# Kernel tuning notes

Hardware: AMD Instinct MI355X
Metric: run time of the kernel (lower is better)

## Reference

```python
import jax, jax.numpy as jnp
import numpy as np

SIM_THRESHOLD = 0.5   # similarity_threshold
LAMBDA = 0.1          # lambda_weight default


def setup_inputs() -> dict:
    key = jax.random.key(0)
    ks = jax.random.split(key, 8)
    B, T, C, P = 8, 1024, 1024, 100
    return {
        "attention_scores": jax.random.normal(ks[0], (B, T, T), jnp.float32),
        "context": jax.random.normal(ks[1], (B, C), jnp.float32),
        "triggers": jax.random.normal(ks[2], (P, C), jnp.float32),
        "biases": jax.random.uniform(ks[3], (P, T, T), jnp.float32),
        "confidences": jnp.ones((P,), jnp.float32),
        "W1": jax.random.normal(ks[4], (2 * C, C), jnp.float32) * (1.0 / np.sqrt(2 * C)),
        "b1": jnp.zeros((C,), jnp.float32),
        "W2": jax.random.normal(ks[5], (C,), jnp.float32) * (1.0 / np.sqrt(C)),
        "b2": jnp.zeros((1,), jnp.float32),
    }


def reference(attention_scores, context, triggers, biases, confidences, W1, b1, W2, b2):
    C = context.shape[-1]
    # combined = cat([context, trigger]) @ W1 == context @ W1[:C] + trigger @ W1[C:]
    ctx_h = context @ W1[:C]              # (B, C)
    trg_h = triggers @ W1[C:]             # (P, C)
    h = jax.nn.relu(ctx_h[:, None, :] + trg_h[None, :, :] + b1)   # (B, P, C)
    logits = h @ W2 + b2[0]               # (B, P)
    scores = jax.nn.sigmoid(logits).mean(axis=0)                  # (P,) mean over batch
    # match: only patterns with score > threshold contribute, weighted by score*confidence
    weights = jnp.where(scores > SIM_THRESHOLD, scores * confidences, 0.0)  # (P,)
    reasoning_bias = jnp.einsum("p,pij->ij", weights, biases)     # (T, T)
    return attention_scores + LAMBDA * reasoning_bias[None, :, :]
```

## Files before the change

kernel.cpp:

```cpp
#include <hip/hip_runtime.h>
#include <hip/hip_bf16.h>
#include <math.h>

#define BD 8
#define TD 1024
#define CD 1024
#define PD 100
#define KS 16
#define KW (CD / KS)
#define LAMBDA 0.1f
#define SIM_THR 0.5f

typedef float f2 __attribute__((ext_vector_type(2)));
typedef float f4 __attribute__((ext_vector_type(4)));

__device__ float    g_pctx[KS][BD][CD];
__device__ float    g_ptrg[KS][PD][CD];
__device__ float    g_wd[PD];
__device__ float    g_wc[PD];
__device__ unsigned g_poff[PD];
__device__ int      g_nnz;

__global__ __launch_bounds__(256) void hidden_kernel(const float* __restrict__ context,
                                                     const float* __restrict__ triggers,
                                                     const float* __restrict__ W1) {
    const int c  = blockIdx.x * 256 + threadIdx.x;
    const int kz = blockIdx.z;
    const int k0 = kz * KW;
    const bool is_ctx = (blockIdx.y == 0);
    const int  ych = blockIdx.y - 1;
    const float* __restrict__ W1p = is_ctx ? W1 : (W1 + (size_t)CD * CD);
    const float* __restrict__ src = is_ctx ? context : (triggers + (size_t)ych * 10 * CD);
    float* __restrict__ dst = is_ctx ? &g_pctx[kz][0][0] : &g_ptrg[kz][ych * 10][0];
    const int nrows = is_ctx ? 8 : 10;

    __shared__ float s_src[10][KW];
    for (int t = threadIdx.x; t < 10 * KW; t += 256) {
        const int r = t >> 6, k = t & (KW - 1);
        s_src[r][k] = src[(size_t)(r < nrows ? r : 0) * CD + k0 + k];
    }
    __syncthreads();

    float acc[10];
#pragma unroll
    for (int i = 0; i < 10; ++i) acc[i] = 0.f;

#pragma unroll 8
    for (int kk = 0; kk < KW; ++kk) {
        const float wv = W1p[(size_t)(k0 + kk) * CD + c];
#pragma unroll
        for (int i = 0; i < 10; ++i)
            acc[i] = fmaf(s_src[i][kk], wv, acc[i]);
    }
#pragma unroll
    for (int i = 0; i < 10; ++i)
        if (i < nrows) dst[(size_t)i * CD + c] = acc[i];
}

__global__ __launch_bounds__(512) void score_kernel(const float* __restrict__ b1,
                                                    const float* __restrict__ W2,
                                                    const float* __restrict__ b2,
                                                    const float* __restrict__ conf) {
    const int p = blockIdx.x;
    __shared__ float s_h[CD];
    __shared__ float s_logit[BD];

    for (int c = threadIdx.x; c < CD; c += 512) {
        float v = b1[c];
#pragma unroll
        for (int kz = 0; kz < KS; ++kz) v += g_ptrg[kz][p][c];
        s_h[c] = v;
    }
    __syncthreads();

    const int b = threadIdx.x >> 6, lane = threadIdx.x & 63;
    float sum = 0.f;
    for (int c = lane; c < CD; c += 64) {
        float v = s_h[c];
#pragma unroll
        for (int kz = 0; kz < KS; ++kz) v += g_pctx[kz][b][c];
        sum = fmaf(fmaxf(v, 0.f), W2[c], sum);
    }
#pragma unroll
    for (int off = 32; off > 0; off >>= 1) sum += __shfl_down(sum, off);
    if (lane == 0) s_logit[b] = sum + b2[0];
    __syncthreads();
    if (threadIdx.x == 0) {
        float s = 0.f;
#pragma unroll
        for (int bb = 0; bb < BD; ++bb) s += 1.f / (1.f + expf(-s_logit[bb]));
        s *= (1.f / BD);
        g_wd[p] = (s > SIM_THR) ? s * conf[p] * LAMBDA : 0.f;
    }
}

__global__ void compact_kernel() {
    if (threadIdx.x == 0) {
        int n = 0;
        for (int q = 0; q < PD; ++q) {
            const float w = g_wd[q];
            if (w != 0.f) {
                g_wc[n]   = w;
                g_poff[n] = (unsigned)(q * (TD * TD));
                ++n;
            }
        }
        g_nnz = n;
    }
}

__global__ __launch_bounds__(256, 8) void out_kernel(const float* __restrict__ attn,
                                                     const float* __restrict__ biases,
                                                     float* __restrict__ out) {
    __shared__ float    s_w[PD];
    __shared__ unsigned s_off[PD];
    const int n = g_nnz;
    if (threadIdx.x < n) {
        s_w[threadIdx.x]   = g_wc[threadIdx.x];
        s_off[threadIdx.x] = g_poff[threadIdx.x];
    }
    __syncthreads();

    const size_t base = (size_t)blockIdx.x * 512 + (size_t)threadIdx.x * 2;

    f2 av[BD];
#pragma unroll
    for (int b = 0; b < BD; ++b)
        av[b] = *(const f2*)(attn + (size_t)b * TD * TD + base);

    f2 acc = {0.f, 0.f};
    int t = 0;
    for (; t + 4 <= n; t += 4) {
        const float w0 = s_w[t + 0], w1 = s_w[t + 1], w2 = s_w[t + 2], w3 = s_w[t + 3];
        const f2 v0 = *(const f2*)(biases + (size_t)s_off[t + 0] + base);
        const f2 v1 = *(const f2*)(biases + (size_t)s_off[t + 1] + base);
        const f2 v2 = *(const f2*)(biases + (size_t)s_off[t + 2] + base);
        const f2 v3 = *(const f2*)(biases + (size_t)s_off[t + 3] + base);
        acc.x = fmaf(w0, v0.x, fmaf(w1, v1.x, fmaf(w2, v2.x, fmaf(w3, v3.x, acc.x))));
        acc.y = fmaf(w0, v0.y, fmaf(w1, v1.y, fmaf(w2, v2.y, fmaf(w3, v3.y, acc.y))));
    }
    for (; t < n; ++t) {
        const float w = s_w[t];
        const f2 bv = *(const f2*)(biases + (size_t)s_off[t] + base);
        acc.x = fmaf(w, bv.x, acc.x);
        acc.y = fmaf(w, bv.y, acc.y);
    }

#pragma unroll
    for (int b = 0; b < BD; ++b) {
        f2 ov = av[b] + acc;
        __builtin_nontemporal_store(ov, (f2*)(out + (size_t)b * TD * TD + base));
    }
}

extern "C" void kernel_launch(void* const* d_in, const int* in_sizes, int n_in,
                              void* d_out, int out_size, void* d_ws, size_t ws_size,
                              hipStream_t stream) {
    const float* attn     = (const float*)d_in[0];
    const float* context  = (const float*)d_in[1];
    const float* triggers = (const float*)d_in[2];
    const float* biases   = (const float*)d_in[3];
    const float* conf     = (const float*)d_in[4];
    const float* W1       = (const float*)d_in[5];
    const float* b1       = (const float*)d_in[6];
    const float* W2       = (const float*)d_in[7];
    const float* b2       = (const float*)d_in[8];
    float* out = (float*)d_out;

    hipLaunchKernelGGL(hidden_kernel, dim3(CD / 256, 11, KS), dim3(256), 0, stream,
                       context, triggers, W1);
    hipLaunchKernelGGL(score_kernel, dim3(PD), dim3(512), 0, stream, b1, W2, b2, conf);
    hipLaunchKernelGGL(compact_kernel, dim3(1), dim3(64), 0, stream);
    hipLaunchKernelGGL(out_kernel, dim3(2048), dim3(256), 0, stream, attn, biases, out);
}
```

Baseline: 109.5 us.

## Split bias patterns across waves per block with LDS reduction and wider loads

The output kernel now gives each block a 2048-element segment and lets its four waves each handle a strided subset of the active patterns. Each lane loads eight float4s of bias per pattern, and the per-wave partial sums are reduced through shared memory before being added to the eight batch slices of attention. The goal is more memory-level parallelism and wider vector loads for the bias stream, which dominates traffic, with fewer blocks each doing more work. In exchange it adds an LDS buffer and a barrier, uses more registers, drops the occupancy hint, and the attention loads no longer overlap with the bias loop.

```diff
diff --git a/kernel.cpp b/kernel.cpp
--- a/kernel.cpp
+++ b/kernel.cpp
@@ -8,10 +8,10 @@
 #define PD 100
 #define KS 16
 #define KW (CD / KS)
+#define SEG 2048
 #define LAMBDA 0.1f
 #define SIM_THR 0.5f
 
-typedef float f2 __attribute__((ext_vector_type(2)));
 typedef float f4 __attribute__((ext_vector_type(4)));
 
 __device__ float    g_pctx[KS][BD][CD];
@@ -109,11 +109,12 @@
     }
 }
 
-__global__ __launch_bounds__(256, 8) void out_kernel(const float* __restrict__ attn,
-                                                     const float* __restrict__ biases,
-                                                     float* __restrict__ out) {
+__global__ __launch_bounds__(256) void out_kernel(const float* __restrict__ attn,
+                                                  const float* __restrict__ biases,
+                                                  float* __restrict__ out) {
     __shared__ float    s_w[PD];
     __shared__ unsigned s_off[PD];
+    __shared__ float    s_part[4][SEG];
     const int n = g_nnz;
     if (threadIdx.x < n) {
         s_w[threadIdx.x]   = g_wc[threadIdx.x];
@@ -121,35 +122,48 @@
     }
     __syncthreads();
 
-    const size_t base = (size_t)blockIdx.x * 512 + (size_t)threadIdx.x * 2;
+    const int wv = threadIdx.x >> 6, lane = threadIdx.x & 63;
+    const size_t seg = (size_t)blockIdx.x * SEG;
 
-    f2 av[BD];
+    f4 acc[8];
 #pragma unroll
-    for (int b = 0; b < BD; ++b)
-        av[b] = *(const f2*)(attn + (size_t)b * TD * TD + base);
+    for (int j = 0; j < 8; ++j) acc[j] = (f4){0.f, 0.f, 0.f, 0.f};
 
-    f2 acc = {0.f, 0.f};
-    int t = 0;
-    for (; t + 4 <= n; t += 4) {
-        const float w0 = s_w[t + 0], w1 = s_w[t + 1], w2 = s_w[t + 2], w3 = s_w[t + 3];
-        const f2 v0 = *(const f2*)(biases + (size_t)s_off[t + 0] + base);
-        const f2 v1 = *(const f2*)(biases + (size_t)s_off[t + 1] + base);
-        const f2 v2 = *(const f2*)(biases + (size_t)s_off[t + 2] + base);
-        const f2 v3 = *(const f2*)(biases + (size_t)s_off[t + 3] + base);
-        acc.x = fmaf(w0, v0.x, fmaf(w1, v1.x, fmaf(w2, v2.x, fmaf(w3, v3.x, acc.x))));
-        acc.y = fmaf(w0, v0.y, fmaf(w1, v1.y, fmaf(w2, v2.y, fmaf(w3, v3.y, acc.y))));
+    for (int t = wv; t < n; t += 4) {
+        const float w = s_w[t];
+        const float* bp = biases + (size_t)s_off[t] + seg + (size_t)lane * 4;
+        f4 v[8];
+#pragma unroll
+        for (int j = 0; j < 8; ++j) v[j] = *(const f4*)(bp + j * 256);
+#pragma unroll
+        for (int j = 0; j < 8; ++j) {
+            acc[j].x = fmaf(w, v[j].x, acc[j].x);
+            acc[j].y = fmaf(w, v[j].y, acc[j].y);
+            acc[j].z = fmaf(w, v[j].z, acc[j].z);
+            acc[j].w = fmaf(w, v[j].w, acc[j].w);
+        }
     }
-    for (; t < n; ++t) {
-        const float w = s_w[t];
-        const f2 bv = *(const f2*)(biases + (size_t)s_off[t] + base);
-        acc.x = fmaf(w, bv.x, acc.x);
-        acc.y = fmaf(w, bv.y, acc.y);
+
+#pragma unroll
+    for (int j = 0; j < 8; ++j)
+        *(f4*)&s_part[wv][j * 256 + lane * 4] = acc[j];
+    __syncthreads();
+
+    const int e = threadIdx.x * 8;
+    f4 r0 = (f4){0.f, 0.f, 0.f, 0.f}, r1 = r0;
+#pragma unroll
+    for (int w2 = 0; w2 < 4; ++w2) {
+        r0 += *(const f4*)&s_part[w2][e];
+        r1 += *(const f4*)&s_part[w2][e + 4];
     }
 
 #pragma unroll
     for (int b = 0; b < BD; ++b) {
-        f2 ov = av[b] + acc;
-        __builtin_nontemporal_store(ov, (f2*)(out + (size_t)b * TD * TD + base));
+        const size_t off = (size_t)b * TD * TD + seg + (size_t)e;
+        const f4 a0 = *(const f4*)(attn + off);
+        const f4 a1 = *(const f4*)(attn + off + 4);
+        __builtin_nontemporal_store(a0 + r0, (f4*)(out + off));
+        __builtin_nontemporal_store(a1 + r1, (f4*)(out + off + 4));
     }
 }
 
@@ -171,5 +185,5 @@
                        context, triggers, W1);
     hipLaunchKernelGGL(score_kernel, dim3(PD), dim3(512), 0, stream, b1, W2, b2, conf);
     hipLaunchKernelGGL(compact_kernel, dim3(1), dim3(64), 0, stream);
-    hipLaunchKernelGGL(out_kernel, dim3(2048), dim3(256), 0, stream, attn, biases, out);
+    hipLaunchKernelGGL(out_kernel, dim3(TD * TD / SEG), dim3(256), 0, stream, attn, biases, out);
 }
```

Result: no change. 111.1 us (+1.5%).
